# Performance work log

Hardware: AMD Instinct MI355X
Metric: run time of the kernel (lower is better)

## Reference

```python
import jax, jax.numpy as jnp
import numpy as np

EPS_LN = 1e-5  # torch nn.LayerNorm default

def layernorm(x, g, b):
    mu = x.mean(-1, keepdims=True)
    var = ((x - mu) ** 2).mean(-1, keepdims=True)
    return (x - mu) * jax.lax.rsqrt(var + EPS_LN) * g + b

def softmax_kernel(x, proj, is_query, kernel_eps=1e-4):
    # FAVOR+ positive softmax random features (performer_pytorch math).
    # x: (B,H,N,D) queries/keys, proj: (M,D) random projection.
    d = x.shape[-1]
    norm = d ** -0.25
    ratio = proj.shape[0] ** -0.5
    xd = jnp.einsum('bhnd,md->bhnm', x * norm, proj)
    diag = 0.5 * (x ** 2).sum(-1, keepdims=True) * (norm ** 2)  # (B,H,N,1)
    stab = jnp.max(xd, axis=-1, keepdims=True) if is_query else jnp.max(xd)
    return ratio * (jnp.exp(xd - diag - stab) + kernel_eps)

def linear_attention(q, k, v):
    # Non-causal O(N) attention. q,k: (B,H,N,M); v: (B,H,N,DH)
    k_sum = k.sum(axis=-2)                                      # (B,H,M)
    d_inv = 1.0 / jnp.einsum('bhnm,bhm->bhn', q, k_sum)
    context = jnp.einsum('bhnm,bhnd->bhmd', k, v)               # (B,H,M,DH)
    return jnp.einsum('bhnm,bhmd,bhn->bhnd', q, context, d_inv)

def setup_inputs():
    key = jax.random.key(0)
    B, K, D, H, L = 32, 2048, 256, 4, 2
    DH = D // H
    M = int(DH * np.log(DH))  # 266, performer_pytorch default nb_features
    FF = 4 * D
    ks = jax.random.split(key, 20)
    def w(i, shape):
        return jax.random.normal(ks[i], shape, dtype=jnp.float32) * 0.02
    return dict(
        expr=jax.random.uniform(ks[0], (B, K), dtype=jnp.float32),
        coords=jax.random.uniform(ks[1], (B, 2), dtype=jnp.float32),
        gene_emb=w(2, (K, D)), pos_emb=w(3, (K, D)),
        val_w=w(4, (1, D)), val_b=jnp.zeros((D,), jnp.float32),
        val_ln_g=jnp.ones((D,), jnp.float32), val_ln_b=jnp.zeros((D,), jnp.float32),
        sp_w=w(5, (2, D)), sp_b=jnp.zeros((D,), jnp.float32),
        sp_ln_g=jnp.ones((D,), jnp.float32), sp_ln_b=jnp.zeros((D,), jnp.float32),
        p_ln1_g=jnp.ones((L, D), jnp.float32), p_ln1_b=jnp.zeros((L, D), jnp.float32),
        p_wq=w(6, (L, D, D)), p_bq=jnp.zeros((L, D), jnp.float32),
        p_wk=w(7, (L, D, D)), p_bk=jnp.zeros((L, D), jnp.float32),
        p_wv=w(8, (L, D, D)), p_bv=jnp.zeros((L, D), jnp.float32),
        p_wo=w(9, (L, D, D)), p_bo=jnp.zeros((L, D), jnp.float32),
        p_ln2_g=jnp.ones((L, D), jnp.float32), p_ln2_b=jnp.zeros((L, D), jnp.float32),
        p_ff1_w=w(10, (L, D, FF)), p_ff1_b=jnp.zeros((L, FF), jnp.float32),
        p_ff2_w=w(11, (L, FF, D)), p_ff2_b=jnp.zeros((L, D), jnp.float32),
        proj=jax.random.normal(ks[12], (L, M, DH), dtype=jnp.float32),
        q_w=w(13, (D, D)), q_b=jnp.zeros((D,), jnp.float32),
        k_w=w(14, (D, D)), k_b=jnp.zeros((D,), jnp.float32),
        v_w=w(15, (D, D)), v_b=jnp.zeros((D,), jnp.float32),
        o_w=w(16, (D, D)), o_b=jnp.zeros((D,), jnp.float32),
    )

def reference(expr, coords, gene_emb, pos_emb, val_w, val_b, val_ln_g, val_ln_b,
              sp_w, sp_b, sp_ln_g, sp_ln_b,
              p_ln1_g, p_ln1_b, p_wq, p_bq, p_wk, p_bk, p_wv, p_bv, p_wo, p_bo,
              p_ln2_g, p_ln2_b, p_ff1_w, p_ff1_b, p_ff2_w, p_ff2_b, proj,
              q_w, q_b, k_w, k_b, v_w, v_b, o_w, o_b):
    B, K = expr.shape
    D = gene_emb.shape[1]
    L = p_wq.shape[0]
    H = 4
    DH = D // H
    # gene tokens = gene_id_emb + gene_pos_emb + GELU(LN(Linear(expr)))
    val = jax.nn.gelu(layernorm(expr[..., None] * val_w[0] + val_b, val_ln_g, val_ln_b), approximate=False)
    gene_tokens = (gene_emb + pos_emb)[None] + val                      # (B,K,D)
    sp = jax.nn.gelu(layernorm(coords @ sp_w + sp_b, sp_ln_g, sp_ln_b), approximate=False)
    x = jnp.concatenate([sp[:, None, :], gene_tokens], axis=1)          # (B,K+1,D)
    N = K + 1
    def split_heads(t):
        return t.reshape(B, N, H, DH).transpose(0, 2, 1, 3)
    # Performer: depth x [x + Attn(LN(x)); x + FF(LN(x))], dropout off (eval)
    for l in range(L):
        y = layernorm(x, p_ln1_g[l], p_ln1_b[l])
        q = split_heads(y @ p_wq[l] + p_bq[l])
        k = split_heads(y @ p_wk[l] + p_bk[l])
        v = split_heads(y @ p_wv[l] + p_bv[l])
        qf = softmax_kernel(q, proj[l], True)
        kf = softmax_kernel(k, proj[l], False)
        o = linear_attention(qf, kf, v)                                 # (B,H,N,DH)
        o = o.transpose(0, 2, 1, 3).reshape(B, N, D)
        x = x + (o @ p_wo[l] + p_bo[l])
        y = layernorm(x, p_ln2_g[l], p_ln2_b[l])
        x = x + (jax.nn.gelu(y @ p_ff1_w[l] + p_ff1_b[l], approximate=False) @ p_ff2_w[l] + p_ff2_b[l])
    # single-query cross-attention pooling: spatial token attends to genes
    spatial_out = x[:, :1]
    gene_out = x[:, 1:]
    q = spatial_out @ q_w + q_b                                          # (B,1,D)
    kk = gene_out @ k_w + k_b                                            # (B,K,D)
    vv = gene_out @ v_w + v_b
    attn = jax.nn.softmax(jnp.einsum('bqd,bkd->bqk', q, kk) / (D ** 0.5), axis=-1)
    pooled = jnp.einsum('bqk,bkd->bqd', attn, vv)[:, 0]                  # (B,D)
    return pooled @ o_w + o_b
```

## Files before the change

kernel.cpp:

```cpp
#include <hip/hip_runtime.h>
#include <hip/hip_bf16.h>
#include <math.h>

#define NB   32
#define KG   2048
#define NSEQ 2049
#define DIM  256
#define NH   4
#define DH   64
#define MF   266
#define FFD  1024
#define BN   (NB*NSEQ)
#define FFROWS2 32784
#define NORMC 0.35355339059327376f
#define RATIOC (1.0f/16.309506430300091f)

typedef __attribute__((ext_vector_type(8))) short short8;
typedef __attribute__((ext_vector_type(4))) float f32x4;
#define MFMA16(a,b,c) __builtin_amdgcn_mfma_f32_16x16x32_bf16(a,b,c,0,0,0)

__device__ __forceinline__ short f2b(float f){
  union{ __hip_bfloat16 h; short s;} u; u.h = __float2bfloat16(f); return u.s;
}
__device__ __forceinline__ float b2f(short s){
  union{ short s; __hip_bfloat16 h;} u; u.s = s; return __bfloat162float(u.h);
}
__device__ __forceinline__ float gelu_f(float x){
  return 0.5f*x*(1.0f+erff(x*0.70710678118654752f));
}
__device__ __forceinline__ void gload16(const short* g, short* l){
  __builtin_amdgcn_global_load_lds(
      (const __attribute__((address_space(1))) void*)g,
      (__attribute__((address_space(3))) void*)l, 16, 0, 0);
}
__device__ __forceinline__ float waveSum(float v){
  #pragma unroll
  for(int o=32;o>0;o>>=1) v += __shfl_down(v,o);
  return v;
}
__device__ __forceinline__ float waveMax(float v){
  #pragma unroll
  for(int o=32;o>0;o>>=1) v = fmaxf(v,__shfl_down(v,o));
  return v;
}
__device__ __forceinline__ float xorSum64(float v){
  v += __shfl_xor(v,32); v += __shfl_xor(v,16); v += __shfl_xor(v,8);
  v += __shfl_xor(v,4);  v += __shfl_xor(v,2);  v += __shfl_xor(v,1);
  return v;
}
__device__ __forceinline__ float blockSum256(float v, float* red){
  int lane = threadIdx.x & 63, wid = threadIdx.x >> 6;
  v = waveSum(v);
  __syncthreads();
  if(lane==0) red[wid]=v;
  __syncthreads();
  return red[0]+red[1]+red[2]+red[3];
}
__device__ __forceinline__ float blockMax256(float v, float* red){
  int lane = threadIdx.x & 63, wid = threadIdx.x >> 6;
  v = waveMax(v);
  __syncthreads();
  if(lane==0) red[wid]=v;
  __syncthreads();
  return fmaxf(fmaxf(red[0],red[1]),fmaxf(red[2],red[3]));
}
__device__ __forceinline__ unsigned fenc(float f){
  unsigned u = __float_as_uint(f);
  return (u & 0x80000000u) ? ~u : (u | 0x80000000u);
}
__device__ __forceinline__ float fdec(unsigned u){
  return (u & 0x80000000u) ? __uint_as_float(u & 0x7FFFFFFFu) : __uint_as_float(~u);
}

__global__ __launch_bounds__(256) void embed_kernel(
    const float* __restrict__ expr, const float* __restrict__ coords,
    const float* __restrict__ gene_emb, const float* __restrict__ pos_emb,
    const float* __restrict__ val_w, const float* __restrict__ val_b,
    const float* __restrict__ val_g, const float* __restrict__ val_bb,
    const float* __restrict__ sp_w, const float* __restrict__ sp_b,
    const float* __restrict__ sp_g, const float* __restrict__ sp_bb,
    const float* __restrict__ ln_g, const float* __restrict__ ln_b,
    float* __restrict__ x, short* __restrict__ ybf){
  int w = threadIdx.x >> 6, l = threadIdx.x & 63;
  int row = blockIdx.x*4 + w;
  int b = row / NSEQ, n = row % NSEQ;
  int d0 = l*4;
  float4 v;
  if(n==0){
    float c0 = coords[b*2], c1 = coords[b*2+1];
    float4 w0 = *reinterpret_cast<const float4*>(sp_w + d0);
    float4 w1 = *reinterpret_cast<const float4*>(sp_w + DIM + d0);
    float4 bb = *reinterpret_cast<const float4*>(sp_b + d0);
    v = make_float4(c0*w0.x+c1*w1.x+bb.x, c0*w0.y+c1*w1.y+bb.y,
                    c0*w0.z+c1*w1.z+bb.z, c0*w0.w+c1*w1.w+bb.w);
  } else {
    float e = expr[(size_t)b*KG + (n-1)];
    float4 vw = *reinterpret_cast<const float4*>(val_w + d0);
    float4 vb = *reinterpret_cast<const float4*>(val_b + d0);
    v = make_float4(e*vw.x+vb.x, e*vw.y+vb.y, e*vw.z+vb.z, e*vw.w+vb.w);
  }
  float mu = xorSum64(v.x+v.y+v.z+v.w)*(1.0f/DIM);
  float cx=v.x-mu, cy=v.y-mu, cz=v.z-mu, cw=v.w-mu;
  float var = xorSum64(cx*cx+cy*cy+cz*cz+cw*cw)*(1.0f/DIM);
  float r = rsqrtf(var + 1e-5f);
  float4 g  = (n==0)? *reinterpret_cast<const float4*>(sp_g + d0)
                    : *reinterpret_cast<const float4*>(val_g + d0);
  float4 be = (n==0)? *reinterpret_cast<const float4*>(sp_bb + d0)
                    : *reinterpret_cast<const float4*>(val_bb + d0);
  float4 h = make_float4(gelu_f(cx*r*g.x+be.x), gelu_f(cy*r*g.y+be.y),
                         gelu_f(cz*r*g.z+be.z), gelu_f(cw*r*g.w+be.w));
  if(n!=0){
    float4 ge = *reinterpret_cast<const float4*>(gene_emb + (size_t)(n-1)*DIM + d0);
    float4 pe = *reinterpret_cast<const float4*>(pos_emb  + (size_t)(n-1)*DIM + d0);
    h.x += ge.x+pe.x; h.y += ge.y+pe.y; h.z += ge.z+pe.z; h.w += ge.w+pe.w;
  }
  *reinterpret_cast<float4*>(x + (size_t)row*DIM + d0) = h;
  float s2 = xorSum64(h.x+h.y+h.z+h.w);
  float mu2 = s2*(1.0f/DIM);
  float c2x=h.x-mu2, c2y=h.y-mu2, c2z=h.z-mu2, c2w=h.w-mu2;
  float var2 = xorSum64(c2x*c2x+c2y*c2y+c2z*c2z+c2w*c2w)*(1.0f/DIM);
  float r2 = rsqrtf(var2+1e-5f);
  const float4 gv = *reinterpret_cast<const float4*>(ln_g + d0);
  const float4 bv = *reinterpret_cast<const float4*>(ln_b + d0);
  short4 o = make_short4(f2b(c2x*r2*gv.x+bv.x), f2b(c2y*r2*gv.y+bv.y),
                         f2b(c2z*r2*gv.z+bv.z), f2b(c2w*r2*gv.w+bv.w));
  *reinterpret_cast<short4*>(ybf + (size_t)row*DIM + d0) = o;
}

__global__ __launch_bounds__(256) void ln_bf4(const float* __restrict__ xin,
    const float* __restrict__ g, const float* __restrict__ bb, short* __restrict__ ybf){
  int w = threadIdx.x >> 6, l = threadIdx.x & 63;
  int row = blockIdx.x*4 + w;
  const float* xr = xin + (size_t)row*DIM;
  float4 v = *reinterpret_cast<const float4*>(xr + l*4);
  float s = xorSum64(v.x+v.y+v.z+v.w);
  float mu = s*(1.0f/DIM);
  float cx=v.x-mu, cy=v.y-mu, cz=v.z-mu, cw=v.w-mu;
  float var = xorSum64(cx*cx+cy*cy+cz*cz+cw*cw)*(1.0f/DIM);
  float r = rsqrtf(var+1e-5f);
  const float4 gv = *reinterpret_cast<const float4*>(g + l*4);
  const float4 bv = *reinterpret_cast<const float4*>(bb + l*4);
  short4 o = make_short4(f2b(cx*r*gv.x+bv.x), f2b(cy*r*gv.y+bv.y),
                         f2b(cz*r*gv.z+bv.z), f2b(cw*r*gv.w+bv.w));
  *reinterpret_cast<short4*>(ybf + (size_t)row*DIM + l*4) = o;
}

#define NW 14
struct WPArgs {
  const float* src[NW];
  short* dst[NW];
  int K[NW], N[NW];
  int ts[NW+1];
};
__global__ __launch_bounds__(256) void wprep_fused(WPArgs a){
  __shared__ float tile[32][33];
  int bx = blockIdx.x, t = threadIdx.x;
  int i = 0;
  while(bx >= a.ts[i+1]) i++;
  int tl = bx - a.ts[i];
  int N = a.N[i], K = a.K[i];
  int tcols = N >> 5;
  int tr = tl / tcols, tc = tl - tr*tcols;
  const float* src = a.src[i];
  short* dst = a.dst[i];
  int r = t>>3, c4 = (t&7)*4;
  float4 v = *reinterpret_cast<const float4*>(src + (size_t)(tr*32+r)*N + tc*32 + c4);
  tile[r][c4+0]=v.x; tile[r][c4+1]=v.y; tile[r][c4+2]=v.z; tile[r][c4+3]=v.w;
  __syncthreads();
  short4 o = make_short4(f2b(tile[c4+0][r]), f2b(tile[c4+1][r]),
                         f2b(tile[c4+2][r]), f2b(tile[c4+3][r]));
  *reinterpret_cast<short4*>(dst + (size_t)(tc*32+r)*K + tr*32 + c4) = o;
}

template<int EPI, int OBF, int WBF>
__global__ __launch_bounds__(256) void mgemm2(
    const short* __restrict__ A, const short* __restrict__ Bt,
    const float* __restrict__ bias, void* __restrict__ Cv,
    int M, int N, int Kd, short* __restrict__ Yb){
  __shared__ short As[128*64];
  __shared__ short Bs[128*64];
  int t=threadIdx.x, l=t&63, w=t>>6, lr=l&15, lk=l>>4;
  int wm=w>>1, wn=w&1;
  int m0=blockIdx.y*128, n0=blockIdx.x*128;
  f32x4 acc[4][4];
  #pragma unroll
  for(int i=0;i<4;i++)
    #pragma unroll
    for(int j=0;j<4;j++) acc[i][j]=f32x4{0.f,0.f,0.f,0.f};
  int rsw = (l>>3)&7;
  for(int k0=0;k0<Kd;k0+=64){
    #pragma unroll
    for(int p=0;p<4;p++){
      int chunk = p*256 + t;
      int row = chunk>>3, qc = chunk&7;
      short* lbase = &As[(size_t)(p*256 + w*64)*8];
      gload16(A + (size_t)(m0+row)*Kd + k0 + (qc^rsw)*8, lbase);
    }
    #pragma unroll
    for(int p=0;p<4;p++){
      int chunk = p*256 + t;
      int row = chunk>>3, qc = chunk&7;
      short* lbase = &Bs[(size_t)(p*256 + w*64)*8];
      gload16(Bt + (size_t)(n0+row)*Kd + k0 + (qc^rsw)*8, lbase);
    }
    __syncthreads();
    #pragma unroll
    for(int ks=0;ks<2;ks++){
      short8 af[4], bfr[4];
      #pragma unroll
      for(int i=0;i<4;i++)
        af[i] = *reinterpret_cast<const short8*>(&As[(wm*64+i*16+lr)*64 + ((ks*32+lk*8)^((lr&7)<<3))]);
      #pragma unroll
      for(int j=0;j<4;j++)
        bfr[j] = *reinterpret_cast<const short8*>(&Bs[(wn*64+j*16+lr)*64 + ((ks*32+lk*8)^((lr&7)<<3))]);
      #pragma unroll
      for(int i=0;i<4;i++)
        #pragma unroll
        for(int j=0;j<4;j++) acc[i][j] = MFMA16(af[i], bfr[j], acc[i][j]);
    }
    __syncthreads();
  }
  #pragma unroll
  for(int i=0;i<4;i++){
    int gm0 = m0 + wm*64 + i*16 + lk*4;
    #pragma unroll
    for(int j=0;j<4;j++){
      int gc = n0 + wn*64 + j*16 + lr;
      float bs = bias[gc];
      #pragma unroll
      for(int r=0;r<4;r++){
        int gm = gm0 + r;
        if(gm<M){
          float vv = acc[i][j][r] + bs;
          if(EPI==2) vv = gelu_f(vv);
          size_t idx = (size_t)gm*N + gc;
          if(OBF){
            ((short*)Cv)[idx] = f2b(vv);
          } else {
            float* C = (float*)Cv;
            if(EPI==1) vv += C[idx];
            C[idx] = vv;
            if(WBF) Yb[idx] = f2b(vv);
          }
        }
      }
    }
  }
}

__global__ __launch_bounds__(256) void qkv_gemm(
    const short* __restrict__ A, const short* __restrict__ Bt,
    const float* __restrict__ bq, const float* __restrict__ bk, const float* __restrict__ bv,
    short* __restrict__ qd, short* __restrict__ kd, short* __restrict__ vd,
    float* __restrict__ diagk, int M){
  __shared__ short As[128*64];
  __shared__ short Bs[128*64];
  int t=threadIdx.x, l=t&63, w=t>>6, lr=l&15, lk=l>>4;
  int wm=w>>1, wn=w&1;
  int m0=blockIdx.y*128, n0=blockIdx.x*128;
  f32x4 acc[4][4];
  #pragma unroll
  for(int i=0;i<4;i++)
    #pragma unroll
    for(int j=0;j<4;j++) acc[i][j]=f32x4{0.f,0.f,0.f,0.f};
  int rsw = (l>>3)&7;
  for(int k0=0;k0<DIM;k0+=64){
    #pragma unroll
    for(int p=0;p<4;p++){
      int chunk = p*256 + t;
      int row = chunk>>3, qc = chunk&7;
      short* lbase = &As[(size_t)(p*256 + w*64)*8];
      gload16(A + (size_t)(m0+row)*DIM + k0 + (qc^rsw)*8, lbase);
    }
    #pragma unroll
    for(int p=0;p<4;p++){
      int chunk = p*256 + t;
      int row = chunk>>3, qc = chunk&7;
      short* lbase = &Bs[(size_t)(p*256 + w*64)*8];
      gload16(Bt + (size_t)(n0+row)*DIM + k0 + (qc^rsw)*8, lbase);
    }
    __syncthreads();
    #pragma unroll
    for(int ks=0;ks<2;ks++){
      short8 af[4], bfr[4];
      #pragma unroll
      for(int i=0;i<4;i++)
        af[i] = *reinterpret_cast<const short8*>(&As[(wm*64+i*16+lr)*64 + ((ks*32+lk*8)^((lr&7)<<3))]);
      #pragma unroll
      for(int j=0;j<4;j++)
        bfr[j] = *reinterpret_cast<const short8*>(&Bs[(wn*64+j*16+lr)*64 + ((ks*32+lk*8)^((lr&7)<<3))]);
      #pragma unroll
      for(int i=0;i<4;i++)
        #pragma unroll
        for(int j=0;j<4;j++) acc[i][j] = MFMA16(af[i], bfr[j], acc[i][j]);
    }
    __syncthreads();
  }
  bool isK = (blockIdx.x==2) || (blockIdx.x==3);
  int headq = ((n0 + wn*64) - 256) >> 6;
  #pragma unroll
  for(int i=0;i<4;i++){
    int gm0 = m0 + wm*64 + i*16 + lk*4;
    float sq[4] = {0.f,0.f,0.f,0.f};
    #pragma unroll
    for(int j=0;j<4;j++){
      int gc = n0 + wn*64 + j*16 + lr;
      int sel = gc >> 8, col = gc & 255;
      short* dst = (sel==0)? qd : ((sel==1)? kd : vd);
      const float* bp = (sel==0)? bq : ((sel==1)? bk : bv);
      float bs = bp[col];
      #pragma unroll
      for(int r=0;r<4;r++){
        int gm = gm0 + r;
        if(gm<M){
          short sv = f2b(acc[i][j][r] + bs);
          dst[(size_t)gm*DIM + col] = sv;
          if(isK){ float kv = b2f(sv); sq[r] += kv*kv; }
        }
      }
    }
    if(isK){
      #pragma unroll
      for(int r=0;r<4;r++){
        float s = sq[r];
        s += __shfl_xor(s,1); s += __shfl_xor(s,2);
        s += __shfl_xor(s,4); s += __shfl_xor(s,8);
        if(lr==0){
          int gm = gm0 + r;
          if(gm<M){
            int bb_ = gm / NSEQ, nn_ = gm - bb_*NSEQ;
            diagk[((size_t)(bb_*NH+headq))*NSEQ + nn_] = 0.0625f*s;
          }
        }
      }
    }
  }
}

__global__ __launch_bounds__(256) void projprep_kernel(const float* __restrict__ proj,
    short* __restrict__ projbf, unsigned* __restrict__ kmax){
  int i = blockIdx.x*256 + threadIdx.x;
  if(i==0) *kmax = 0u;
  if(i < 320*64){
    int m = i>>6, d = i&63;
    float v = (m<MF)? proj[(size_t)m*DH + d]*NORMC : 0.f;
    projbf[i] = f2b(v);
  }
}

__global__ __launch_bounds__(256) void kside_max(
    const short* __restrict__ kbf, const short* __restrict__ projbf,
    unsigned* __restrict__ kmax){
  __shared__ short kS[64*64];
  __shared__ float red[4];
  int t=threadIdx.x, l=t&63, w=t>>6, lr=l&15, lk=l>>4;
  int split = blockIdx.x, bh = blockIdx.y;
  int b=bh>>2, h=bh&3;
  int c0 = split*5, c1 = min(c0+5, 33);
  int nf = (w==3)?5:4;
  short8 apf[5][2];
  #pragma unroll
  for(int fi=0;fi<5;fi++){
    int fr = (fi<4)? (fi*4+w) : 16;
    #pragma unroll
    for(int ks=0;ks<2;ks++)
      apf[fi][ks] = *reinterpret_cast<const short8*>(projbf + (fr*16+lr)*64 + ks*32 + lk*8);
  }
  int rsw = (l>>3)&7;
  float lmax = -3.0e38f;
  for(int ch=c0; ch<c1; ++ch){
    int n0 = ch*64;
    __syncthreads();
    #pragma unroll
    for(int p=0;p<2;p++){
      int chunk = p*256 + t;
      int row = chunk>>3, qc = chunk&7;
      short* lbase = &kS[(size_t)(p*256 + w*64)*8];
      gload16(kbf + (size_t)(b*NSEQ + n0 + row)*DIM + h*DH + (qc^rsw)*8, lbase);
    }
    __syncthreads();
    for(int fi=0;fi<nf;fi++){
      int fr = (fi<4)? (fi*4+w) : 16;
      #pragma unroll
      for(int fn=0;fn<4;fn++){
        f32x4 xa = f32x4{0.f,0.f,0.f,0.f};
        #pragma unroll
        for(int ks=0;ks<2;ks++){
          short8 bk = *reinterpret_cast<const short8*>(&kS[(fn*16+lr)*64 + ((ks*32+lk*8)^((lr&7)<<3))]);
          xa = MFMA16(apf[fi][ks], bk, xa);
        }
        #pragma unroll
        for(int r=0;r<4;r++){
          int m = fr*16 + lk*4 + r;
          int n = n0 + fn*16 + lr;
          if(m<MF && n<NSEQ) lmax = fmaxf(lmax, xa[r]);
        }
      }
    }
  }
  float bm = blockMax256(lmax, red);
  if(t==0) atomicMax(kmax, fenc(bm));
}

__global__ __launch_bounds__(256) void kside_ctx(
    const short* __restrict__ kbf, const short* __restrict__ vbf,
    const short* __restrict__ projbf, const float* __restrict__ diagk,
    const unsigned* __restrict__ kmax, float* __restrict__ ctxP){
  __shared__ short kS[64*64];
  __shared__ short vT[64*72];
  __shared__ short kfS[80*72];
  __shared__ float diagS[64];
  int t=threadIdx.x, l=t&63, w=t>>6, lr=l&15, lk=l>>4;
  int fb=blockIdx.x&3, qh=blockIdx.x>>2, bh=blockIdx.y; int b=bh>>2, h=bh&3;
  int F0 = fb*5;
  int ch0 = qh*17, ch1 = min(33, ch0+17);
  float stab = fdec(*kmax);
  short8 apf0[2], apf1[2];
  #pragma unroll
  for(int ks=0;ks<2;ks++){
    apf0[ks] = *reinterpret_cast<const short8*>(projbf + ((F0+w)*16+lr)*64 + ks*32 + lk*8);
    apf1[ks] = *reinterpret_cast<const short8*>(projbf + ((F0+4)*16+lr)*64 + ks*32 + lk*8);
  }
  f32x4 ctx[5];
  #pragma unroll
  for(int f=0;f<5;f++) ctx[f]=f32x4{0.f,0.f,0.f,0.f};
  f32x4 ksc0 = f32x4{0.f,0.f,0.f,0.f};
  f32x4 ksc1 = f32x4{0.f,0.f,0.f,0.f};
  const short ONE=(short)0x3F80;
  const short8 ones8 = {ONE,ONE,ONE,ONE,ONE,ONE,ONE,ONE};
  int rsw = (l>>3)&7;
  for(int ch=ch0; ch<ch1; ++ch){
    int n0 = ch*64;
    __syncthreads();
    #pragma unroll
    for(int p=0;p<2;p++){
      int chunk = p*256 + t;
      int row = chunk>>3, qc = chunk&7;
      short* lbase = &kS[(size_t)(p*256 + w*64)*8];
      gload16(kbf + (size_t)(b*NSEQ + n0 + row)*DIM + h*DH + (qc^rsw)*8, lbase);
    }
    #pragma unroll
    for(int p=0;p<8;p++){
      int n2 = 2*w + 8*p;
      int dd = l;
      int gn0=n0+n2, gn1=gn0+1;
      short v0 = (gn0<NSEQ)? vbf[((size_t)(b*NSEQ+gn0))*DIM + h*DH + dd] : (short)0;
      short v1 = (gn1<NSEQ)? vbf[((size_t)(b*NSEQ+gn1))*DIM + h*DH + dd] : (short)0;
      *reinterpret_cast<short2*>(&vT[dd*72 + n2]) = make_short2(v0,v1);
    }
    if(t<64) diagS[t] = (n0+t<NSEQ)? diagk[(size_t)bh*NSEQ + n0+t] : 0.f;
    __syncthreads();
    #pragma unroll
    for(int fn=0;fn<4;fn++){
      f32x4 xa = f32x4{0.f,0.f,0.f,0.f};
      #pragma unroll
      for(int ks=0;ks<2;ks++){
        short8 bk = *reinterpret_cast<const short8*>(&kS[(fn*16+lr)*64 + ((ks*32+lk*8)^((lr&7)<<3))]);
        xa = MFMA16(apf0[ks], bk, xa);
      }
      float dgn = diagS[fn*16+lr];
      #pragma unroll
      for(int r=0;r<4;r++){
        int m = (F0+w)*16 + lk*4 + r;
        int n = n0 + fn*16 + lr;
        float kf = (m<MF && n<NSEQ)? RATIOC*(__expf(xa[r]-dgn-stab)+1e-4f) : 0.f;
        kfS[(w*16+lk*4+r)*72 + fn*16 + lr] = f2b(kf);
      }
    }
    if(w==0){
      #pragma unroll
      for(int fn=0;fn<4;fn++){
        f32x4 xa = f32x4{0.f,0.f,0.f,0.f};
        #pragma unroll
        for(int ks=0;ks<2;ks++){
          short8 bk = *reinterpret_cast<const short8*>(&kS[(fn*16+lr)*64 + ((ks*32+lk*8)^((lr&7)<<3))]);
          xa = MFMA16(apf1[ks], bk, xa);
        }
        float dgn = diagS[fn*16+lr];
        #pragma unroll
        for(int r=0;r<4;r++){
          int m = (F0+4)*16 + lk*4 + r;
          int n = n0 + fn*16 + lr;
          float kf = (m<MF && n<NSEQ)? RATIOC*(__expf(xa[r]-dgn-stab)+1e-4f) : 0.f;
          kfS[(64+lk*4+r)*72 + fn*16 + lr] = f2b(kf);
        }
      }
    }
    __syncthreads();
    #pragma unroll
    for(int ks2=0;ks2<2;ks2++){
      short8 bv = *reinterpret_cast<const short8*>(&vT[(w*16+lr)*72 + ks2*32 + lk*8]);
      short8 a0 = *reinterpret_cast<const short8*>(&kfS[(w*16+lr)*72 + ks2*32 + lk*8]);
      short8 a4 = *reinterpret_cast<const short8*>(&kfS[(64+lr)*72 + ks2*32 + lk*8]);
      ksc0 = MFMA16(a0, ones8, ksc0);
      ksc1 = MFMA16(a4, ones8, ksc1);
      #pragma unroll
      for(int fl=0;fl<5;fl++){
        short8 a_ = *reinterpret_cast<const short8*>(&kfS[(fl*16+lr)*72 + ks2*32 + lk*8]);
        ctx[fl] = MFMA16(a_, bv, ctx[fl]);
      }
    }
  }
  float* P = ctxP + ((size_t)(qh*128 + bh))*65*320;
  #pragma unroll
  for(int fl=0;fl<5;fl++){
    #pragma unroll
    for(int r=0;r<4;r++){
      int m = (F0+fl)*16 + lk*4 + r;
      P[(size_t)(w*16+lr)*320 + m] = ctx[fl][r];
    }
  }
  if(lr==0){
    #pragma unroll
    for(int r=0;r<4;r++){
      int m = (F0+w)*16 + lk*4 + r;
      P[(size_t)64*320 + m] = ksc0[r];
    }
    if(w==0){
      #pragma unroll
      for(int r=0;r<4;r++){
        int m = (F0+4)*16 + lk*4 + r;
        P[(size_t)64*320 + m] = ksc1[r];
      }
    }
  }
}

__global__ __launch_bounds__(256) void ctx_reduce(const float* __restrict__ ctxP, short* __restrict__ ctxT){
  int row = blockIdx.x, bh = blockIdx.y, t = threadIdx.x;
  short* o = ctxT + ((size_t)bh*80 + row)*288;
  if(row < 65){
    const float* P0 = ctxP + ((size_t)bh*65 + row)*320;
    const float* P1 = ctxP + ((size_t)(128+bh)*65 + row)*320;
    for(int m=t; m<288; m+=256)
      o[m] = (m<272)? f2b(P0[m]+P1[m]) : (short)0;
  } else {
    for(int m=t; m<288; m+=256) o[m] = 0;
  }
}

__global__ __launch_bounds__(256) void qside_mfma(
    const short* __restrict__ qbf, const short* __restrict__ projbf,
    const short* __restrict__ ctxT, short* __restrict__ obf){
  __shared__ short qfS[64*296];
  __shared__ float diagS[64];
  short* qS = qfS;
  int t=threadIdx.x, l=t&63, w=t>>6, lr=l&15, lk=l>>4;
  int n0 = blockIdx.x*64, bh = blockIdx.y;
  int b = bh>>2, h = bh&3;
  const short8 z8 = {0,0,0,0,0,0,0,0};
  {
    int r = t>>2, c8 = (t&3)*16;
    int gn = n0 + r;
    float ssq = 0.f;
    #pragma unroll
    for(int i=0;i<2;i++){
      short8 v8 = z8;
      if(gn<NSEQ) v8 = *reinterpret_cast<const short8*>(qbf + ((size_t)(b*NSEQ+gn))*DIM + h*DH + c8 + i*8);
      #pragma unroll
      for(int u=0;u<8;u++){ float fv=b2f(v8[u]); ssq += fv*fv; }
      *reinterpret_cast<short8*>(&qS[r*72+c8+i*8]) = v8;
    }
    ssq += __shfl_xor(ssq,1); ssq += __shfl_xor(ssq,2);
    if((t&3)==0) diagS[r] = 0.0625f*ssq;
  }
  short8 aq[2];
  #pragma unroll
  for(int ks=0;ks<2;ks++) aq[ks] = *reinterpret_cast<const short8*>(&qS[(w*16+lr)*72 + ks*32 + lk*8]);
  float dg[4];
  #pragma unroll
  for(int r=0;r<4;r++) dg[r] = diagS[w*16 + lk*4 + r];
  __syncthreads();
  {
    int pr = w*16 + (l>>2), pc = 272 + (l&3)*4;
    #pragma unroll
    for(int i=0;i<4;i++) qfS[pr*296 + pc + i] = 0;
  }
  f32x4 acc[17];
  #pragma unroll
  for(int f=0;f<17;f++) acc[f]=f32x4{0.f,0.f,0.f,0.f};
  #pragma unroll
  for(int f=0;f<17;f++){
    #pragma unroll
    for(int ks=0;ks<2;ks++){
      short8 bp = *reinterpret_cast<const short8*>(projbf + (f*16+lr)*64 + ks*32 + lk*8);
      acc[f] = MFMA16(aq[ks], bp, acc[f]);
    }
  }
  float rmax[4];
  #pragma unroll
  for(int r=0;r<4;r++){
    float m = -3.0e38f;
    #pragma unroll
    for(int f=0;f<17;f++){
      float v = (f==16 && lr>=10)? -3.0e38f : acc[f][r];
      m = fmaxf(m,v);
    }
    m = fmaxf(m,__shfl_xor(m,1)); m = fmaxf(m,__shfl_xor(m,2));
    m = fmaxf(m,__shfl_xor(m,4)); m = fmaxf(m,__shfl_xor(m,8));
    rmax[r]=m;
  }
  #pragma unroll
  for(int f=0;f<17;f++)
    #pragma unroll
    for(int r=0;r<4;r++){
      float qv = RATIOC*(__expf(acc[f][r] - dg[r] - rmax[r]) + 1e-4f);
      qfS[(w*16+lk*4+r)*296 + f*16 + lr] = f2b(qv);
    }
  f32x4 pv[5];
  #pragma unroll
  for(int f=0;f<5;f++) pv[f]=f32x4{0.f,0.f,0.f,0.f};
  const short* cT = ctxT + (size_t)bh*80*288;
  for(int ks=0;ks<9;ks++){
    short8 a_ = *reinterpret_cast<const short8*>(&qfS[(w*16+lr)*296 + ks*32 + lk*8]);
    #pragma unroll
    for(int f=0;f<5;f++){
      short8 bb = *reinterpret_cast<const short8*>(cT + (f*16+lr)*288 + ks*32 + lk*8);
      pv[f] = MFMA16(a_, bb, pv[f]);
    }
  }
  #pragma unroll
  for(int r=0;r<4;r++){
    int gn = n0 + w*16 + lk*4 + r;
    if(gn>=NSEQ) continue;
    float den = __shfl(pv[4][r], (l & 48), 64);
    float inv = 1.0f/den;
    size_t obase = ((size_t)(b*NSEQ+gn))*DIM + h*DH;
    #pragma unroll
    for(int f=0;f<4;f++) obf[obase + f*16 + lr] = f2b(pv[f][r]*inv);
  }
}

__global__ __launch_bounds__(256) void rowproj_kernel(const float* __restrict__ src,
    const float* __restrict__ W, const float* __restrict__ bias,
    float* __restrict__ dst, int rowstride){
  __shared__ float rs[DIM];
  int b=blockIdx.x, t=threadIdx.x;
  rs[t]=src[(size_t)b*rowstride+t];
  __syncthreads();
  float s=bias[t];
  for(int j=0;j<DIM;j++) s += rs[j]*W[(size_t)j*DIM+t];
  dst[(size_t)b*DIM+t]=s;
}

__global__ __launch_bounds__(256) void pool_scores(const float* __restrict__ qfin,
    const short* __restrict__ kk, float* __restrict__ scb){
  __shared__ float qsh[DIM];
  int kc=blockIdx.x, b=blockIdx.y, t=threadIdx.x;
  qsh[t]=qfin[b*DIM+t];
  __syncthreads();
  int kidx = kc*256 + t;
  const short* kr = kk + ((size_t)(b*NSEQ+1+kidx))*DIM;
  float s=0;
  for(int j8=0;j8<32;j8++){
    short8 kv = *reinterpret_cast<const short8*>(kr + j8*8);
    #pragma unroll
    for(int u=0;u<8;u++) s += qsh[j8*8+u]*b2f(kv[u]);
  }
  scb[(size_t)b*KG + kidx] = s*0.0625f;
}

__global__ __launch_bounds__(256) void pool_sm(const float* __restrict__ scb,
    float* __restrict__ gms){
  __shared__ float red[4];
  int b=blockIdx.x, t=threadIdx.x;
  float ls[8]; float lmax=-3.4e38f;
  #pragma unroll
  for(int i=0;i<8;i++){
    ls[i] = scb[(size_t)b*KG + t + i*256];
    lmax = fmaxf(lmax, ls[i]);
  }
  float gmax=blockMax256(lmax,red);
  float lsum=0;
  #pragma unroll
  for(int i=0;i<8;i++) lsum += __expf(ls[i]-gmax);
  float gsum=blockSum256(lsum,red);
  if(t==0){ gms[b*2]=gmax; gms[b*2+1]=gsum; }
}

__global__ __launch_bounds__(256) void pool_pv2(const float* __restrict__ scb,
    const float* __restrict__ gms, const short* __restrict__ vv,
    float* __restrict__ part){
  __shared__ float es[256];
  int kc=blockIdx.x, b=blockIdx.y, t=threadIdx.x;
  float gmax = gms[b*2];
  es[t] = __expf(scb[(size_t)b*KG + kc*256 + t] - gmax);
  __syncthreads();
  float p=0;
  for(int i=0;i<256;i++){
    int kidx = kc*256 + i;
    p += es[i] * b2f(vv[((size_t)(b*NSEQ+1+kidx))*DIM + t]);
  }
  part[((size_t)(b*8)+kc)*DIM + t] = p;
}

__global__ __launch_bounds__(256) void pool_fin(const float* __restrict__ part,
    const float* __restrict__ gms, float* __restrict__ pooled){
  int b=blockIdx.x, t=threadIdx.x;
  float inv = 1.0f/gms[b*2+1];
  float s=0;
  #pragma unroll
  for(int kc=0;kc<8;kc++) s += part[((size_t)(b*8)+kc)*DIM + t];
  pooled[b*DIM+t] = s*inv;
}

extern "C" void kernel_launch(void* const* d_in, const int* in_sizes, int n_in,
                              void* d_out, int out_size, void* d_ws, size_t ws_size,
                              hipStream_t stream){
  const float* expr   =(const float*)d_in[0];
  const float* coords =(const float*)d_in[1];
  const float* gene_emb=(const float*)d_in[2];
  const float* pos_emb=(const float*)d_in[3];
  const float* val_w  =(const float*)d_in[4];
  const float* val_b  =(const float*)d_in[5];
  const float* val_g  =(const float*)d_in[6];
  const float* val_bb =(const float*)d_in[7];
  const float* sp_w   =(const float*)d_in[8];
  const float* sp_b   =(const float*)d_in[9];
  const float* sp_g   =(const float*)d_in[10];
  const float* sp_bb  =(const float*)d_in[11];
  const float* p_ln1_g=(const float*)d_in[12];
  const float* p_ln1_b=(const float*)d_in[13];
  const float* p_wq   =(const float*)d_in[14];
  const float* p_bq   =(const float*)d_in[15];
  const float* p_wk   =(const float*)d_in[16];
  const float* p_bk   =(const float*)d_in[17];
  const float* p_wv   =(const float*)d_in[18];
  const float* p_bv   =(const float*)d_in[19];
  const float* p_wo   =(const float*)d_in[20];
  const float* p_bo   =(const float*)d_in[21];
  const float* p_ln2_g=(const float*)d_in[22];
  const float* p_ln2_b=(const float*)d_in[23];
  const float* p_ff1_w=(const float*)d_in[24];
  const float* p_ff1_b=(const float*)d_in[25];
  const float* p_ff2_w=(const float*)d_in[26];
  const float* p_ff2_b=(const float*)d_in[27];
  const float* proj   =(const float*)d_in[28];
  const float* q_w    =(const float*)d_in[29];
  const float* q_b    =(const float*)d_in[30];
  const float* k_w    =(const float*)d_in[31];
  const float* k_b    =(const float*)d_in[32];
  const float* v_w    =(const float*)d_in[33];
  const float* v_b    =(const float*)d_in[34];
  const float* o_w    =(const float*)d_in[35];
  const float* o_b    =(const float*)d_in[36];
  float* out = (float*)d_out;

  const size_t BND = (size_t)BN*DIM;
  size_t needB = BND*4 + BND*2*4
               + ((size_t)NB*NH*NSEQ + 4 + 2*(size_t)NB*DIM)*4
               + ((size_t)20480 + 2949120 + 1703936)*2;
  if(ws_size < needB){
    hipMemsetAsync(d_out, 0, (size_t)out_size*sizeof(float), stream);
    return;
  }
  float* ws = (float*)d_ws;
  float* x  = ws;
  short* ybf = (short*)(x + BND);
  short* qbf = ybf + BND;
  short* kbf = qbf + BND;
  short* vbf = kbf + BND;
  float* diagk = (float*)(vbf + BND);
  unsigned* kmax = (unsigned*)(diagk + (size_t)NB*NH*NSEQ);
  float* qfin   = (float*)(kmax+4);
  float* pooled = qfin + NB*DIM;
  short* projbf = (short*)(pooled + NB*DIM);
  short* ctxT   = projbf + 20480;
  short* wt     = ctxT + (size_t)128*80*288;
  const size_t LW = 786432;
  float* ctxP = (float*)ybf;
  float* scb  = diagk;
  float* gms  = diagk + 65536;
  float* ppart= gms + 64;

  {
    WPArgs a;
    short* wtkk = wt + 2*LW;
    short* wtvv = wtkk + 65536;
    const float* s10[10] = {p_wq, p_wk, p_wv, p_wo,
                            p_wq+(size_t)DIM*DIM, p_wk+(size_t)DIM*DIM,
                            p_wv+(size_t)DIM*DIM, p_wo+(size_t)DIM*DIM,
                            k_w, v_w};
    short* d10[10] = {wt, wt+65536, wt+131072, wt+196608,
                      wt+LW, wt+LW+65536, wt+LW+131072, wt+LW+196608,
                      wtkk, wtvv};
    int ti = 0;
    for(int i=0;i<10;i++){
      a.src[i]=s10[i]; a.dst[i]=d10[i]; a.K[i]=DIM; a.N[i]=DIM;
      a.ts[i]=ti; ti+=64;
    }
    const float* sff[4] = {p_ff1_w, p_ff2_w, p_ff1_w+(size_t)DIM*FFD, p_ff2_w+(size_t)FFD*DIM};
    short* dff[4] = {wt+262144, wt+524288, wt+LW+262144, wt+LW+524288};
    int Kff[4] = {DIM, FFD, DIM, FFD};
    int Nff[4] = {FFD, DIM, FFD, DIM};
    for(int i=0;i<4;i++){
      a.src[10+i]=sff[i]; a.dst[10+i]=dff[i]; a.K[10+i]=Kff[i]; a.N[10+i]=Nff[i];
      a.ts[10+i]=ti; ti+=256;
    }
    a.ts[14]=ti;
    wprep_fused<<<1664,256,0,stream>>>(a);
  }

  embed_kernel<<<BN/4,256,0,stream>>>(expr,coords,gene_emb,pos_emb,val_w,val_b,val_g,val_bb,
                                      sp_w,sp_b,sp_g,sp_bb, p_ln1_g, p_ln1_b, x, ybf);

  dim3 gdd(2, (BN+127)/128);
  dim3 gqkv(6, (BN+127)/128);
  dim3 gff1(8, (FFROWS2+127)/128);
  dim3 gff2(2, (FFROWS2+127)/128);
  dim3 gkm(7, NB*NH);
  dim3 gkc(8, NB*NH);
  dim3 gcr(80, NB*NH);
  dim3 gq((NSEQ+63)/64, NB*NH);
  dim3 gps(8, NB);
  short* wtkk = wt + 2*LW;
  short* wtvv = wtkk + 65536;

  for(int l=0;l<2;l++){
    short* wl = wt + (size_t)l*LW;
    if(l>0) ln_bf4<<<BN/4,256,0,stream>>>(x, p_ln1_g+l*DIM, p_ln1_b+l*DIM, ybf);
    qkv_gemm<<<gqkv,256,0,stream>>>(ybf, wl, p_bq+l*DIM, p_bk+l*DIM, p_bv+l*DIM,
                                    qbf, kbf, vbf, diagk, BN);
    projprep_kernel<<<80,256,0,stream>>>(proj + (size_t)l*MF*DH, projbf, kmax);
    kside_max<<<gkm,256,0,stream>>>(kbf, projbf, kmax);
    kside_ctx<<<gkc,256,0,stream>>>(kbf, vbf, projbf, diagk, kmax, ctxP);
    ctx_reduce<<<gcr,256,0,stream>>>(ctxP, ctxT);
    qside_mfma<<<gq,256,0,stream>>>(qbf, projbf, ctxT, kbf);
    mgemm2<1,0,0><<<gdd,256,0,stream>>>(kbf, wl+196608, p_bo+l*DIM, x, BN, DIM, DIM, nullptr);
    ln_bf4<<<BN/4,256,0,stream>>>(x, p_ln2_g+l*DIM, p_ln2_b+l*DIM, ybf);
    for(int c2=0;c2<2;c2++){
      size_t roff=(size_t)c2*FFROWS2;
      mgemm2<2,1,0><<<gff1,256,0,stream>>>(ybf+roff*DIM, wl+262144, p_ff1_b+l*FFD, qbf,
                                           FFROWS2, FFD, DIM, nullptr);
      if(l==1)
        mgemm2<1,0,1><<<gff2,256,0,stream>>>(qbf, wl+524288, p_ff2_b+l*DIM, x+roff*DIM,
                                             FFROWS2, DIM, FFD, ybf+roff*DIM);
      else
        mgemm2<1,0,0><<<gff2,256,0,stream>>>(qbf, wl+524288, p_ff2_b+l*DIM, x+roff*DIM,
                                             FFROWS2, DIM, FFD, nullptr);
    }
  }

  mgemm2<0,1,0><<<gdd,256,0,stream>>>(ybf, wtkk, k_b, kbf, BN, DIM, DIM, nullptr);
  mgemm2<0,1,0><<<gdd,256,0,stream>>>(ybf, wtvv, v_b, vbf, BN, DIM, DIM, nullptr);
  rowproj_kernel<<<NB,256,0,stream>>>(x, q_w, q_b, qfin, NSEQ*DIM);
  pool_scores<<<gps,256,0,stream>>>(qfin, kbf, scb);
  pool_sm<<<NB,256,0,stream>>>(scb, gms);
  pool_pv2<<<gps,256,0,stream>>>(scb, gms, vbf, ppart);
  pool_fin<<<NB,256,0,stream>>>(ppart, gms, pooled);
  rowproj_kernel<<<NB,256,0,stream>>>(pooled, o_w, o_b, out, DIM);
}
```

Before: 1.417 ms.

## Add XCD-aware block swizzle to GEMM/attention kernels and XOR-swizzle kside_ctx LDS

Adds an XCD-aware remapping of workgroup indices so that consecutive logical tiles land on the same chiplet. The remapping is applied to the GEMMs, qkv_gemm, kside_max, kside_ctx and qside_mfma, with the aim of improving L2 reuse across the eight XCDs. It also replaces the padded (stride 72) LDS layouts for vT and kfS in kside_ctx with an unpadded stride-64 XOR-swizzled layout, to avoid bank conflicts and shrink LDS use. The risks are indexing errors in the swizzled store and load addresses, and a small amount of extra integer work per block.

```diff
diff --git a/kernel.cpp b/kernel.cpp
--- a/kernel.cpp
+++ b/kernel.cpp
@@ -32,6 +32,15 @@
   __builtin_amdgcn_global_load_lds(
       (const __attribute__((address_space(1))) void*)g,
       (__attribute__((address_space(3))) void*)l, 16, 0, 0);
+}
+__device__ __forceinline__ void xcd_swz(int &bx, int &by){
+  int nx = gridDim.x;
+  int nwg = nx * gridDim.y;
+  int flat = by*nx + bx;
+  int q = nwg >> 3, r = nwg & 7;
+  int x = flat & 7, base = flat >> 3;
+  int swz = (x < r ? x*(q+1) : r*(q+1) + (x-r)*q) + base;
+  bx = swz % nx; by = swz / nx;
 }
 __device__ __forceinline__ float waveSum(float v){
   #pragma unroll
@@ -181,7 +190,9 @@
   __shared__ short Bs[128*64];
   int t=threadIdx.x, l=t&63, w=t>>6, lr=l&15, lk=l>>4;
   int wm=w>>1, wn=w&1;
-  int m0=blockIdx.y*128, n0=blockIdx.x*128;
+  int bx = blockIdx.x, by = blockIdx.y;
+  xcd_swz(bx, by);
+  int m0=by*128, n0=bx*128;
   f32x4 acc[4][4];
   #pragma unroll
   for(int i=0;i<4;i++)
@@ -257,7 +268,9 @@
   __shared__ short Bs[128*64];
   int t=threadIdx.x, l=t&63, w=t>>6, lr=l&15, lk=l>>4;
   int wm=w>>1, wn=w&1;
-  int m0=blockIdx.y*128, n0=blockIdx.x*128;
+  int bx = blockIdx.x, by = blockIdx.y;
+  xcd_swz(bx, by);
+  int m0=by*128, n0=bx*128;
   f32x4 acc[4][4];
   #pragma unroll
   for(int i=0;i<4;i++)
@@ -296,7 +309,7 @@
     }
     __syncthreads();
   }
-  bool isK = (blockIdx.x==2) || (blockIdx.x==3);
+  bool isK = (bx==2) || (bx==3);
   int headq = ((n0 + wn*64) - 256) >> 6;
   #pragma unroll
   for(int i=0;i<4;i++){
@@ -355,6 +368,7 @@
   __shared__ float red[4];
   int t=threadIdx.x, l=t&63, w=t>>6, lr=l&15, lk=l>>4;
   int split = blockIdx.x, bh = blockIdx.y;
+  xcd_swz(split, bh);
   int b=bh>>2, h=bh&3;
   int c0 = split*5, c1 = min(c0+5, 33);
   int nf = (w==3)?5:4;
@@ -407,11 +421,13 @@
     const short* __restrict__ projbf, const float* __restrict__ diagk,
     const unsigned* __restrict__ kmax, float* __restrict__ ctxP){
   __shared__ short kS[64*64];
-  __shared__ short vT[64*72];
-  __shared__ short kfS[80*72];
+  __shared__ short vT[64*64];
+  __shared__ short kfS[80*64];
   __shared__ float diagS[64];
   int t=threadIdx.x, l=t&63, w=t>>6, lr=l&15, lk=l>>4;
-  int fb=blockIdx.x&3, qh=blockIdx.x>>2, bh=blockIdx.y; int b=bh>>2, h=bh&3;
+  int bxx = blockIdx.x, byy = blockIdx.y;
+  xcd_swz(bxx, byy);
+  int fb=bxx&3, qh=bxx>>2, bh=byy; int b=bh>>2, h=bh&3;
   int F0 = fb*5;
   int ch0 = qh*17, ch1 = min(33, ch0+17);
   float stab = fdec(*kmax);
@@ -446,7 +462,7 @@
       int gn0=n0+n2, gn1=gn0+1;
       short v0 = (gn0<NSEQ)? vbf[((size_t)(b*NSEQ+gn0))*DIM + h*DH + dd] : (short)0;
       short v1 = (gn1<NSEQ)? vbf[((size_t)(b*NSEQ+gn1))*DIM + h*DH + dd] : (short)0;
-      *reinterpret_cast<short2*>(&vT[dd*72 + n2]) = make_short2(v0,v1);
+      *reinterpret_cast<short2*>(&vT[dd*64 + (p^(dd&7))*8 + 2*w]) = make_short2(v0,v1);
     }
     if(t<64) diagS[t] = (n0+t<NSEQ)? diagk[(size_t)bh*NSEQ + n0+t] : 0.f;
     __syncthreads();
@@ -464,7 +480,9 @@
         int m = (F0+w)*16 + lk*4 + r;
         int n = n0 + fn*16 + lr;
         float kf = (m<MF && n<NSEQ)? RATIOC*(__expf(xa[r]-dgn-stab)+1e-4f) : 0.f;
-        kfS[(w*16+lk*4+r)*72 + fn*16 + lr] = f2b(kf);
+        int rowm = w*16 + lk*4 + r;
+        int dc = fn*2 + (lr>>3);
+        kfS[rowm*64 + ((dc^((lk*4+r)&7))<<3) + (lr&7)] = f2b(kf);
       }
     }
     if(w==0){
@@ -482,21 +500,24 @@
           int m = (F0+4)*16 + lk*4 + r;
           int n = n0 + fn*16 + lr;
           float kf = (m<MF && n<NSEQ)? RATIOC*(__expf(xa[r]-dgn-stab)+1e-4f) : 0.f;
-          kfS[(64+lk*4+r)*72 + fn*16 + lr] = f2b(kf);
+          int rowm = 64 + lk*4 + r;
+          int dc = fn*2 + (lr>>3);
+          kfS[rowm*64 + ((dc^((lk*4+r)&7))<<3) + (lr&7)] = f2b(kf);
         }
       }
     }
     __syncthreads();
     #pragma unroll
     for(int ks2=0;ks2<2;ks2++){
-      short8 bv = *reinterpret_cast<const short8*>(&vT[(w*16+lr)*72 + ks2*32 + lk*8]);
-      short8 a0 = *reinterpret_cast<const short8*>(&kfS[(w*16+lr)*72 + ks2*32 + lk*8]);
-      short8 a4 = *reinterpret_cast<const short8*>(&kfS[(64+lr)*72 + ks2*32 + lk*8]);
+      int pc = ((ks2*4+lk)^(lr&7))<<3;
+      short8 bv = *reinterpret_cast<const short8*>(&vT[(w*16+lr)*64 + pc]);
+      short8 a0 = *reinterpret_cast<const short8*>(&kfS[(w*16+lr)*64 + pc]);
+      short8 a4 = *reinterpret_cast<const short8*>(&kfS[(64+lr)*64 + pc]);
       ksc0 = MFMA16(a0, ones8, ksc0);
       ksc1 = MFMA16(a4, ones8, ksc1);
       #pragma unroll
       for(int fl=0;fl<5;fl++){
-        short8 a_ = *reinterpret_cast<const short8*>(&kfS[(fl*16+lr)*72 + ks2*32 + lk*8]);
+        short8 a_ = *reinterpret_cast<const short8*>(&kfS[(fl*16+lr)*64 + pc]);
         ctx[fl] = MFMA16(a_, bv, ctx[fl]);
       }
     }
@@ -546,7 +567,9 @@
   __shared__ float diagS[64];
   short* qS = qfS;
   int t=threadIdx.x, l=t&63, w=t>>6, lr=l&15, lk=l>>4;
-  int n0 = blockIdx.x*64, bh = blockIdx.y;
+  int bxx = blockIdx.x, byy = blockIdx.y;
+  xcd_swz(bxx, byy);
+  int n0 = bxx*64, bh = byy;
   int b = bh>>2, h = bh&3;
   const short8 z8 = {0,0,0,0,0,0,0,0};
   {
```

Measured after the change: 1.451 ms. +2.3%, slower.
